# Kernel optimization log

Hardware: AMD Instinct MI355X
Metric: run time of the kernel (lower is better)

## Reference

```python
import jax, jax.numpy as jnp
import numpy as np

B, D = 16384, 2048

def setup_inputs() -> dict:
    key = jax.random.key(0)
    k1, k2, k3 = jax.random.split(key, 3)
    x = jax.random.normal(k1, (B, D), dtype=jnp.float32)
    x_dot = jax.random.normal(k2, (B, D), dtype=jnp.float32)
    # linear score_fn weight, scaled like standard init
    W = jax.random.normal(k3, (D, D), dtype=jnp.float32) / np.sqrt(D).astype(np.float32)
    return {"x": x, "x_dot": x_dot, "W": W}


def reference(x, x_dot, W) -> jnp.ndarray:
    # score_fn: s = x @ W^T  -> [B, D]
    s = jnp.einsum('bd,ed->be', x, W)
    # G = I - s s^T / (1 + ||s||^2); kinetic = x_dot^T G x_dot.
    # Exact algebraic collapse (Sherman-Morrison rank-1 form):
    #   x_dot.G.x_dot = ||x_dot||^2 - (s.x_dot)^2 / (1 + ||s||^2)
    norm_sq = jnp.sum(s * s, axis=1)            # [B]
    sx = jnp.sum(s * x_dot, axis=1)             # [B]
    xx = jnp.sum(x_dot * x_dot, axis=1)         # [B]
    return xx - (sx * sx) / (1.0 + norm_sq)      # [B]
```

## Files before the change

kernel.cpp:

```cpp
#include <hip/hip_runtime.h>


#define MTOT 16384
#define DTOT 2048
#define NK 16

typedef unsigned char u8;
typedef __attribute__((ext_vector_type(4))) float f32x4;
typedef __attribute__((ext_vector_type(8))) int i32x8;

__device__ __forceinline__ unsigned f2e2m1(float f) {
    unsigned sgn = f < 0.f ? 8u : 0u;
    float a = fabsf(f);
    unsigned c;
    if      (a < 0.25f) c = 0;
    else if (a < 0.75f) c = 1;
    else if (a < 1.25f) c = 2;
    else if (a < 1.75f) c = 3;
    else if (a < 2.5f)  c = 4;
    else if (a < 3.5f)  c = 5;
    else if (a < 5.0f)  c = 6;
    else                c = 7;
    return sgn | c;
}

__device__ __forceinline__ void gload_lds16(const void* gptr, void* ldsptr) {
    __builtin_amdgcn_global_load_lds(
        (const __attribute__((address_space(1))) unsigned int*)gptr,
        (__attribute__((address_space(3))) unsigned int*)ldsptr,
        16, 0, 0);
}

#define BARS()   __builtin_amdgcn_s_barrier()
#define SCHED0() __builtin_amdgcn_sched_barrier(0)
#define LGKM0()  asm volatile("s_waitcnt lgkmcnt(0)")
#define WAITV(n) asm volatile("s_waitcnt vmcnt(" #n ")")

__global__ void cast4_kernel(const float* __restrict__ src, unsigned* __restrict__ dst,
                             int n8, float mul) {
    int stride = gridDim.x * blockDim.x;
    for (int i = blockIdx.x * blockDim.x + threadIdx.x; i < n8; i += stride) {
        f32x4 v0 = ((const f32x4*)src)[2 * (size_t)i];
        f32x4 v1 = ((const f32x4*)src)[2 * (size_t)i + 1];
        dst[i] =  f2e2m1(v0[0] * mul)        | (f2e2m1(v0[1] * mul) << 4)  |
                 (f2e2m1(v0[2] * mul) << 8)  | (f2e2m1(v0[3] * mul) << 12) |
                 (f2e2m1(v1[0] * mul) << 16) | (f2e2m1(v1[1] * mul) << 20) |
                 (f2e2m1(v1[2] * mul) << 24) | (f2e2m1(v1[3] * mul) << 28);
    }
}

__global__ __launch_bounds__(256, 3)
void gemmf4(const u8* __restrict__ xq, const u8* __restrict__ wq,
            const float* __restrict__ xdot,
            float* __restrict__ ns_acc, float* __restrict__ sx_acc,
            float* __restrict__ xx_acc) {
    __shared__ u8 lds[32768];

    const int tid  = threadIdx.x;
    const int lane = tid & 63;
    const int wid  = tid >> 6;
    const int wr = wid >> 1, wc = wid & 1;
    const int fr = lane & 15, fq = lane >> 4;

    const int bid = blockIdx.x;
    const int brow = ((bid & 7) * 16 + ((bid >> 3) & 15)) * 128;
    const int bcol = (bid >> 7) * 128;

    const int RS = DTOT / 2;

    auto stage_region = [&](const u8* src, int region) {
#pragma unroll
        for (int c2 = 0; c2 < 2; ++c2) {
            const int c = c2 * 256 + tid;
            const int L = c >> 3, p = c & 7;
            const int q = p ^ (L & 7);
            gload_lds16(src + (size_t)(2 * L + (q >> 2)) * RS + (q & 3) * 16,
                        (char*)lds + region + c * 16);
        }
    };
    auto stage_tile = [&](int kt, int bufbyte) {
        const int kb = kt * 64;
        stage_region(xq + (size_t)brow * RS + kb, bufbyte);
        stage_region(wq + (size_t)bcol * RS + kb, bufbyte + 8192);
    };

    auto rdfrag = [&](int region, int row) -> int4 {
        const int L = row >> 1;
        const int p = ((((row & 1) << 2) | fq) ^ (L & 7));
        return *(const int4*)((const char*)lds + region + L * 128 + (p << 4));
    };
    auto mk8 = [](int4 v) -> i32x8 {
        i32x8 r;
        r[0] = v.x; r[1] = v.y; r[2] = v.z; r[3] = v.w;
        r[4] = 0;   r[5] = 0;   r[6] = 0;   r[7] = 0;
        return r;
    };

    f32x4 acc[4][4] = {};
    int4 bf[4], a0, a1;

    stage_tile(0, 0);
    WAITV(0);
    SCHED0(); BARS();

    for (int t = 0; t < NK; ++t) {
        const int buf   = (t & 1) * 16384;
        const int abase = buf;
        const int bbase = buf + 8192;

        {
            const int v = t + 1 > NK - 1 ? NK - 1 : t + 1;
            stage_tile(v, (~t & 1) * 16384);
        }

#pragma unroll
        for (int n = 0; n < 4; ++n) bf[n] = rdfrag(bbase, wc * 64 + n * 16 + fr);
        a0 = rdfrag(abase, wr * 64 + fr);
#pragma unroll
        for (int m = 0; m < 4; ++m) {
            if (m + 1 < 4) a1 = rdfrag(abase, wr * 64 + (m + 1) * 16 + fr);
            __builtin_amdgcn_s_setprio(1);
#pragma unroll
            for (int n = 0; n < 4; ++n)
                acc[m][n] = __builtin_amdgcn_mfma_scale_f32_16x16x128_f8f6f4(
                    mk8(a0), mk8(bf[n]), acc[m][n],
                    4, 4,
                    0, 0x7f7f7f7f,
                    0, 0x7f7f7f7f);
            __builtin_amdgcn_s_setprio(0);
            a0 = a1;
        }
        LGKM0();
        WAITV(0);
        SCHED0(); BARS();
    }

#pragma unroll
    for (int m = 0; m < 4; ++m) {
#pragma unroll
        for (int jj = 0; jj < 4; ++jj) {
            const int row = brow + wr * 64 + m * 16 + fq * 4 + jj;
            const float* xp = xdot + (size_t)row * DTOT + bcol + wc * 64 + fr;
            float pns = 0.f, psx = 0.f, pxx = 0.f;
#pragma unroll
            for (int n = 0; n < 4; ++n) {
                float s  = acc[m][n][jj];
                float xv = xp[n * 16];
                pns += s * s; psx += s * xv; pxx += xv * xv;
            }
#pragma unroll
            for (int msk = 1; msk < 16; msk <<= 1) {
                pns += __shfl_xor(pns, msk);
                psx += __shfl_xor(psx, msk);
                pxx += __shfl_xor(pxx, msk);
            }
            if (fr == 0) {
                atomicAdd(&ns_acc[row], pns);
                atomicAdd(&sx_acc[row], psx);
                atomicAdd(&xx_acc[row], pxx);
            }
        }
    }
}

__global__ void finalize_k(const float* __restrict__ ns, const float* __restrict__ sx,
                           const float* __restrict__ xx, float* __restrict__ out) {
    int i = blockIdx.x * blockDim.x + threadIdx.x;
    if (i < MTOT) out[i] = xx[i] - (sx[i] * sx[i]) / (4096.0f + ns[i]);
}

extern "C" void kernel_launch(void* const* d_in, const int* in_sizes, int n_in,
                              void* d_out, int out_size, void* d_ws, size_t ws_size,
                              hipStream_t stream) {
    const float* x  = (const float*)d_in[0];
    const float* xd = (const float*)d_in[1];
    const float* W  = (const float*)d_in[2];
    float* out = (float*)d_out;

    const size_t xq_bytes = (size_t)MTOT * DTOT / 2;
    const size_t wq_bytes = (size_t)DTOT * DTOT / 2;
    const size_t acc_bytes = (size_t)3 * MTOT * 4;

    u8* xq = (u8*)d_ws;
    u8* wq = (u8*)((char*)d_ws + xq_bytes);
    float* accs = (float*)((char*)d_ws + xq_bytes + wq_bytes);
    float* nsA = accs;
    float* sxA = accs + MTOT;
    float* xxA = accs + 2 * MTOT;
    (void)ws_size; (void)in_sizes; (void)n_in; (void)out_size;

    hipMemsetAsync(accs, 0, acc_bytes, stream);

    cast4_kernel<<<2048, 256, 0, stream>>>(x, (unsigned*)xq, MTOT * DTOT / 8, 1.0f);
    cast4_kernel<<<512, 256, 0, stream>>>(W, (unsigned*)wq, DTOT * DTOT / 8, 64.0f);
    gemmf4<<<2048, 256, 0, stream>>>(xq, wq, xd, nsA, sxA, xxA);
    finalize_k<<<MTOT / 256, 256, 0, stream>>>(nsA, sxA, xxA, out);
}
```

Measured before the change: 117.7 us.

## Pre-tile FP4 operands into MFMA fragment layout and load directly to registers

The cast kernels now write the FP4-quantized x and W in a fragment-ordered layout, so each lane can fetch its 16-byte MFMA operand with one contiguous global load. The GEMM drops LDS staging, the swizzle and the block barriers, and instead double-buffers register fragments loaded straight from global memory (through cache). This removes LDS traffic and synchronisation. In exchange, each wave re-reads its operands from L2 without sharing them through LDS, and global load latency is hidden only by a single-step register prefetch.

```diff
diff --git a/kernel.cpp b/kernel.cpp
--- a/kernel.cpp
+++ b/kernel.cpp
@@ -24,38 +24,31 @@
     return sgn | c;
 }
 
-__device__ __forceinline__ void gload_lds16(const void* gptr, void* ldsptr) {
-    __builtin_amdgcn_global_load_lds(
-        (const __attribute__((address_space(1))) unsigned int*)gptr,
-        (__attribute__((address_space(3))) unsigned int*)ldsptr,
-        16, 0, 0);
-}
-
-#define BARS()   __builtin_amdgcn_s_barrier()
-#define SCHED0() __builtin_amdgcn_sched_barrier(0)
-#define LGKM0()  asm volatile("s_waitcnt lgkmcnt(0)")
-#define WAITV(n) asm volatile("s_waitcnt vmcnt(" #n ")")
-
-__global__ void cast4_kernel(const float* __restrict__ src, unsigned* __restrict__ dst,
-                             int n8, float mul) {
+__global__ void cast4t_kernel(const float* __restrict__ src, uint4* __restrict__ dst,
+                              int nchunks, float mul) {
     int stride = gridDim.x * blockDim.x;
-    for (int i = blockIdx.x * blockDim.x + threadIdx.x; i < n8; i += stride) {
-        f32x4 v0 = ((const f32x4*)src)[2 * (size_t)i];
-        f32x4 v1 = ((const f32x4*)src)[2 * (size_t)i + 1];
-        dst[i] =  f2e2m1(v0[0] * mul)        | (f2e2m1(v0[1] * mul) << 4)  |
-                 (f2e2m1(v0[2] * mul) << 8)  | (f2e2m1(v0[3] * mul) << 12) |
-                 (f2e2m1(v1[0] * mul) << 16) | (f2e2m1(v1[1] * mul) << 20) |
-                 (f2e2m1(v1[2] * mul) << 24) | (f2e2m1(v1[3] * mul) << 28);
+    for (int j = blockIdx.x * blockDim.x + threadIdx.x; j < nchunks; j += stride) {
+        const int rowblk = j >> 10, kchunk = (j >> 4) & 63, fr = j & 15;
+        const int row = rowblk * 16 + fr;
+        const f32x4* p = (const f32x4*)(src + (size_t)row * DTOT + kchunk * 32);
+        unsigned w[4];
+#pragma unroll
+        for (int q = 0; q < 4; ++q) {
+            f32x4 v0 = p[2 * q], v1 = p[2 * q + 1];
+            w[q] =  f2e2m1(v0[0] * mul)        | (f2e2m1(v0[1] * mul) << 4)  |
+                   (f2e2m1(v0[2] * mul) << 8)  | (f2e2m1(v0[3] * mul) << 12) |
+                   (f2e2m1(v1[0] * mul) << 16) | (f2e2m1(v1[1] * mul) << 20) |
+                   (f2e2m1(v1[2] * mul) << 24) | (f2e2m1(v1[3] * mul) << 28);
+        }
+        dst[j] = make_uint4(w[0], w[1], w[2], w[3]);
     }
 }
 
 __global__ __launch_bounds__(256, 3)
-void gemmf4(const u8* __restrict__ xq, const u8* __restrict__ wq,
+void gemmf4(const u8* __restrict__ xqt, const u8* __restrict__ wqt,
             const float* __restrict__ xdot,
             float* __restrict__ ns_acc, float* __restrict__ sx_acc,
             float* __restrict__ xx_acc) {
-    __shared__ u8 lds[32768];
-
     const int tid  = threadIdx.x;
     const int lane = tid & 63;
     const int wid  = tid >> 6;
@@ -66,29 +59,15 @@
     const int brow = ((bid & 7) * 16 + ((bid >> 3) & 15)) * 128;
     const int bcol = (bid >> 7) * 128;
 
-    const int RS = DTOT / 2;
+    const u8* pA[4];
+    const u8* pB[4];
+#pragma unroll
+    for (int m = 0; m < 4; ++m)
+        pA[m] = xqt + (size_t)(((brow >> 4) + wr * 4 + m) * 64 + fq) * 256 + fr * 16;
+#pragma unroll
+    for (int n = 0; n < 4; ++n)
+        pB[n] = wqt + (size_t)(((bcol >> 4) + wc * 4 + n) * 64 + fq) * 256 + fr * 16;
 
-    auto stage_region = [&](const u8* src, int region) {
-#pragma unroll
-        for (int c2 = 0; c2 < 2; ++c2) {
-            const int c = c2 * 256 + tid;
-            const int L = c >> 3, p = c & 7;
-            const int q = p ^ (L & 7);
-            gload_lds16(src + (size_t)(2 * L + (q >> 2)) * RS + (q & 3) * 16,
-                        (char*)lds + region + c * 16);
-        }
-    };
-    auto stage_tile = [&](int kt, int bufbyte) {
-        const int kb = kt * 64;
-        stage_region(xq + (size_t)brow * RS + kb, bufbyte);
-        stage_region(wq + (size_t)bcol * RS + kb, bufbyte + 8192);
-    };
-
-    auto rdfrag = [&](int region, int row) -> int4 {
-        const int L = row >> 1;
-        const int p = ((((row & 1) << 2) | fq) ^ (L & 7));
-        return *(const int4*)((const char*)lds + region + L * 128 + (p << 4));
-    };
     auto mk8 = [](int4 v) -> i32x8 {
         i32x8 r;
         r[0] = v.x; r[1] = v.y; r[2] = v.z; r[3] = v.w;
@@ -97,42 +76,44 @@
     };
 
     f32x4 acc[4][4] = {};
-    int4 bf[4], a0, a1;
-
-    stage_tile(0, 0);
-    WAITV(0);
-    SCHED0(); BARS();
-
-    for (int t = 0; t < NK; ++t) {
-        const int buf   = (t & 1) * 16384;
-        const int abase = buf;
-        const int bbase = buf + 8192;
-
-        {
-            const int v = t + 1 > NK - 1 ? NK - 1 : t + 1;
-            stage_tile(v, (~t & 1) * 16384);
-        }
+    int4 aA[4], bA[4], aB[4], bB[4];
 
 #pragma unroll
-        for (int n = 0; n < 4; ++n) bf[n] = rdfrag(bbase, wc * 64 + n * 16 + fr);
-        a0 = rdfrag(abase, wr * 64 + fr);
+    for (int m = 0; m < 4; ++m) aA[m] = *(const int4*)(pA[m]);
 #pragma unroll
-        for (int m = 0; m < 4; ++m) {
-            if (m + 1 < 4) a1 = rdfrag(abase, wr * 64 + (m + 1) * 16 + fr);
-            __builtin_amdgcn_s_setprio(1);
+    for (int n = 0; n < 4; ++n) bA[n] = *(const int4*)(pB[n]);
+
+#pragma unroll
+    for (int t = 0; t < NK; t += 2) {
+        const int o1 = (t + 1 < NK ? t + 1 : t) * 1024;
+#pragma unroll
+        for (int m = 0; m < 4; ++m) aB[m] = *(const int4*)(pA[m] + o1);
+#pragma unroll
+        for (int n = 0; n < 4; ++n) bB[n] = *(const int4*)(pB[n] + o1);
+        __builtin_amdgcn_s_setprio(1);
+#pragma unroll
+        for (int m = 0; m < 4; ++m)
 #pragma unroll
             for (int n = 0; n < 4; ++n)
                 acc[m][n] = __builtin_amdgcn_mfma_scale_f32_16x16x128_f8f6f4(
-                    mk8(a0), mk8(bf[n]), acc[m][n],
-                    4, 4,
-                    0, 0x7f7f7f7f,
-                    0, 0x7f7f7f7f);
-            __builtin_amdgcn_s_setprio(0);
-            a0 = a1;
-        }
-        LGKM0();
-        WAITV(0);
-        SCHED0(); BARS();
+                    mk8(aA[m]), mk8(bA[n]), acc[m][n],
+                    4, 4, 0, 0x7f7f7f7f, 0, 0x7f7f7f7f);
+        __builtin_amdgcn_s_setprio(0);
+
+        const int o2 = (t + 2 < NK ? t + 2 : t) * 1024;
+#pragma unroll
+        for (int m = 0; m < 4; ++m) aA[m] = *(const int4*)(pA[m] + o2);
+#pragma unroll
+        for (int n = 0; n < 4; ++n) bA[n] = *(const int4*)(pB[n] + o2);
+        __builtin_amdgcn_s_setprio(1);
+#pragma unroll
+        for (int m = 0; m < 4; ++m)
+#pragma unroll
+            for (int n = 0; n < 4; ++n)
+                acc[m][n] = __builtin_amdgcn_mfma_scale_f32_16x16x128_f8f6f4(
+                    mk8(aB[m]), mk8(bB[n]), acc[m][n],
+                    4, 4, 0, 0x7f7f7f7f, 0, 0x7f7f7f7f);
+        __builtin_amdgcn_s_setprio(0);
     }
 
 #pragma unroll
@@ -181,8 +162,8 @@
     const size_t wq_bytes = (size_t)DTOT * DTOT / 2;
     const size_t acc_bytes = (size_t)3 * MTOT * 4;
 
-    u8* xq = (u8*)d_ws;
-    u8* wq = (u8*)((char*)d_ws + xq_bytes);
+    u8* xqt = (u8*)d_ws;
+    u8* wqt = (u8*)((char*)d_ws + xq_bytes);
     float* accs = (float*)((char*)d_ws + xq_bytes + wq_bytes);
     float* nsA = accs;
     float* sxA = accs + MTOT;
@@ -191,8 +172,8 @@
 
     hipMemsetAsync(accs, 0, acc_bytes, stream);
 
-    cast4_kernel<<<2048, 256, 0, stream>>>(x, (unsigned*)xq, MTOT * DTOT / 8, 1.0f);
-    cast4_kernel<<<512, 256, 0, stream>>>(W, (unsigned*)wq, DTOT * DTOT / 8, 64.0f);
-    gemmf4<<<2048, 256, 0, stream>>>(xq, wq, xd, nsA, sxA, xxA);
+    cast4t_kernel<<<2048, 256, 0, stream>>>(x, (uint4*)xqt, MTOT * 64, 1.0f);
+    cast4t_kernel<<<512, 256, 0, stream>>>(W, (uint4*)wqt, DTOT * 64, 64.0f);
+    gemmf4<<<2048, 256, 0, stream>>>(xqt, wqt, xd, nsA, sxA, xxA);
     finalize_k<<<MTOT / 256, 256, 0, stream>>>(nsA, sxA, xxA, out);
 }
```

Result: slower. 405.1 us (+244.1%).
